# Kernel optimization log

Hardware: AMD Instinct MI355X
Metric: run time of the kernel (lower is better)

Reference implementation:

```python
import jax, jax.numpy as jnp
import numpy as np

SIGMA = 2.0
EPS = 1e-06
# Truncation radius for the distance transform. exp(-R^2/(2*sigma^2)) = exp(-128)
# underflows to 0.0 in float32, so clipping distances at R reproduces
# scipy.ndimage.distance_transform_edt -> exp(...) exactly in float32.
R = 32


def _boundary_weights(y, sigma=SIGMA, radius=R):
    """y: (B,H,W) binary {0,1}. Returns exp(-d^2/(2 sigma^2)) where d is the
    Euclidean distance to the nearest foreground pixel (0 on FG), computed by
    an exact two-pass separable EDT truncated at `radius` (exact in fp32 after exp)."""
    B, H, W = y.shape
    fg = y > 0.5
    Rf = jnp.float32(radius)
    offs = jnp.arange(-radius, radius + 1)

    # Pass 1 (vertical): g[i,j] = min(radius, min_{i': fg[i',j]} |i-i'|)
    fg_pad = jnp.pad(fg, ((0, 0), (radius, radius), (0, 0)))  # pad with False

    def vstep(g, o):
        sl = jax.lax.dynamic_slice_in_dim(fg_pad, radius + o, H, axis=1)
        g = jnp.minimum(g, jnp.where(sl, jnp.abs(o).astype(jnp.float32), Rf))
        return g, None

    g, _ = jax.lax.scan(vstep, jnp.full((B, H, W), Rf), offs)

    # Pass 2 (horizontal): d2[i,j] = min(radius^2, min_o g[i,j+o]^2 + o^2)
    g2 = g * g
    r2 = float(radius * radius)
    g2_pad = jnp.pad(g2, ((0, 0), (0, 0), (radius, radius)), constant_values=r2)

    def hstep(d2, o):
        sl = jax.lax.dynamic_slice_in_dim(g2_pad, radius + o, W, axis=2)
        d2 = jnp.minimum(d2, sl + (o * o).astype(jnp.float32))
        return d2, None

    d2, _ = jax.lax.scan(hstep, jnp.full((B, H, W), jnp.float32(r2)), offs)
    return jnp.exp(-d2 / (2.0 * sigma * sigma))


def setup_inputs() -> dict:
    key = jax.random.key(0)
    k1, k2 = jax.random.split(key)
    B, C, H, W = 8, 1, 1024, 1024
    probs = jax.random.uniform(k1, (B, C, H, W), dtype=jnp.float32,
                               minval=1e-4, maxval=1.0 - 1e-4)
    targets = (jax.random.uniform(k2, (B, C, H, W)) < 0.02).astype(jnp.float32)
    return {"probs": probs, "targets": targets}


def reference(probs, targets):
    eps = EPS
    y = (targets > 0.5).astype(probs.dtype)                      # (B,1,H,W)
    S_pos = y.sum()
    S_tot = float(y.size)
    S_neg = S_tot - S_pos
    w_pos = jnp.minimum((S_neg + eps) / (S_pos + eps), 1.0)      # scalar
    w_neg_base = (S_pos + eps) / (S_neg + eps)                   # scalar
    w_bdry = _boundary_weights(y[:, 0])[:, None]                 # (B,1,H,W)
    w_neg = jnp.minimum(w_neg_base + w_bdry, 1.0)
    p = jnp.clip(probs, eps, 1.0 - eps)
    loss = w_neg * (1.0 - y) * (-jnp.log1p(-p)) + w_pos * y * (-jnp.log(p))
    return loss.mean()
```

## Files before the change

kernel.cpp:

```cpp
#include <hip/hip_runtime.h>
#include <stdint.h>

#define BB 8
#define HH 1024
#define WW 1024
#define NPIXF 8388608.0f
#define TH 8
#define SROWS 24
#define NRB (HH / TH)
#define NBLK (NRB * BB)
#define GROW 292


__device__ __forceinline__ int phys_idx(int y) { return y + (y >> 3); }

__global__ __launch_bounds__(256, 4) void main_kernel(
    const float* __restrict__ probs,
    const float* __restrict__ targets,
    float4* __restrict__ ws4)
{
    __shared__ uint32_t fgb[SROWS][33];
    __shared__ uint32_t gtw[TH][GROW];
    __shared__ uint32_t redc[4];
    __shared__ float redf[4][3];

    const int t = threadIdx.x;
    const int v = t >> 6, l = t & 63;

    const int L = blockIdx.x + (blockIdx.y << 7);
    const int rb = ((L & 7) << 4) | ((L >> 3) & 15);
    const int b = L >> 7;
    const int r0 = rb * TH;
    const size_t ibase = (size_t)b << 20;

    const uint32_t* tg = (const uint32_t*)(targets + ibase);
    uint32_t cnt = 0;
    #pragma unroll
    for (int q = 0; q < 3; ++q) {
        const int task = q * 256 + t;
        const int r  = task >> 5;
        const int hw = task & 31;
        const int gr = r0 - 8 + r;
        uint32_t w = 0;
        if (gr >= 0 && gr < HH) {
            const uint4* rp = (const uint4*)(tg + ((size_t)gr << 10)) + (hw << 3);
            #pragma unroll
            for (int m = 0; m < 8; ++m) {
                const uint4 u = rp[m];
                const uint32_t nib = ((u.x >> 23) & 1u) | (((u.y >> 23) & 1u) << 1)
                                   | (((u.z >> 23) & 1u) << 2) | (((u.w >> 23) & 1u) << 3);
                w |= nib << (m << 2);
            }
        }
        fgb[r][hw] = w;
        if ((unsigned)(r - 8) < (unsigned)TH) cnt += __popc(w);
    }
    if (t < TH) {
        gtw[t][0] = 0x40404040u; gtw[t][1] = 0x40404040u;
        gtw[t][290] = 0x40404040u; gtw[t][291] = 0x40404040u;
    }
    __syncthreads();

    {
        const int i  = t >> 5;
        const int hw = t & 31;
        uint32_t rbw[15];
        #pragma unroll
        for (int s = 0; s < 15; ++s) rbw[s] = fgb[1 + i + s][hw];
        uint32_t D = rbw[7];
        uint32_t S0 = ~D, S1 = 0, S2 = 0, S3 = 0;
        #pragma unroll
        for (int k = 1; k <= 7; ++k) {
            D |= rbw[7 - k] | rbw[7 + k];
            const uint32_t cc = ~D;
            const uint32_t t0 = S0 & cc; S0 ^= cc;
            const uint32_t t1 = S1 & t0; S1 ^= t0;
            const uint32_t t2 = S2 & t1; S2 ^= t1;
            S3 |= t2;
        }
        #pragma unroll
        for (int m = 0; m < 8; ++m) {
            uint32_t pk = 0;
            #pragma unroll
            for (int c = 0; c < 4; ++c) {
                const int j = (m << 2) | c;
                const uint32_t g = ((S0 >> j) & 1u) | (((S1 >> j) & 1u) << 1)
                                 | (((S2 >> j) & 1u) << 2) | (((S3 >> j) & 1u) << 3);
                pk |= (g * g) << (c << 3);
            }
            const int y = 2 + (hw << 3) + m;
            gtw[i][phys_idx(y)] = pk;
        }
    }
    __syncthreads();

    uint32_t wv[TH][5];
    #pragma unroll
    for (int i = 0; i < TH; ++i) {
        #pragma unroll
        for (int k = 0; k < 5; ++k) wv[i][k] = gtw[i][phys_idx(t + k)];
    }

    float accA = 0.0f, accB = 0.0f, accC = 0.0f;
    const float4* pb = (const float4*)(probs + ibase) + ((size_t)r0 << 8);
    float4 pr = pb[t];
    #pragma unroll
    for (int i = 0; i < TH; ++i) {
        const float4 cur = pr;
        if (i + 1 < TH) pr = pb[((i + 1) << 8) + t];

        int sqb[19];
        #pragma unroll
        for (int rbx = 1; rbx <= 18; ++rbx)
            sqb[rbx] = (int)((wv[i][rbx >> 2] >> ((rbx & 3) << 3)) & 0xFFu);

        const float pv[4] = {cur.x, cur.y, cur.z, cur.w};
        #pragma unroll
        for (int cc = 0; cc < 4; ++cc) {
            int d2 = 64;
            #pragma unroll
            for (int m = 0; m < 15; ++m) {
                const int oc = (m - 7) * (m - 7);
                d2 = min(d2, sqb[cc + m + 1] + oc);
            }
            const float p = pv[cc];
            const bool y = (sqb[cc + 8] == 0);
            const float q = y ? p : (1.0f - p);
            const float L2 = -__logf(q);
            const float wb = __expf(-0.125f * (float)d2);
            const float Lbg = y ? 0.0f : L2;
            accA += (L2 - Lbg);
            accB += Lbg;
            accC = fmaf(wb, Lbg, accC);
        }
    }

    #pragma unroll
    for (int off = 32; off; off >>= 1) {
        accA += __shfl_down(accA, off, 64);
        accB += __shfl_down(accB, off, 64);
        accC += __shfl_down(accC, off, 64);
        cnt  += __shfl_down(cnt,  off, 64);
    }
    if (l == 0) { redc[v] = cnt; redf[v][0] = accA; redf[v][1] = accB; redf[v][2] = accC; }
    __syncthreads();
    if (t == 0) {
        float4 o;
        o.x = (float)(redc[0] + redc[1] + redc[2] + redc[3]);
        o.y = redf[0][0] + redf[1][0] + redf[2][0] + redf[3][0];
        o.z = redf[0][1] + redf[1][1] + redf[2][1] + redf[3][1];
        o.w = redf[0][2] + redf[1][2] + redf[2][2] + redf[3][2];
        ws4[b * NRB + rb] = o;
    }
}

__global__ __launch_bounds__(256) void final_kernel(
    const float4* __restrict__ ws4,
    float* __restrict__ out)
{
    __shared__ float4 red[4];
    const int t = threadIdx.x;
    float4 s = ws4[t];
    #pragma unroll
    for (int k = 1; k < NBLK / 256; ++k) {
        const float4 s2 = ws4[t + k * 256];
        s.x += s2.x; s.y += s2.y; s.z += s2.z; s.w += s2.w;
    }
    #pragma unroll
    for (int off = 32; off; off >>= 1) {
        s.x += __shfl_down(s.x, off, 64);
        s.y += __shfl_down(s.y, off, 64);
        s.z += __shfl_down(s.z, off, 64);
        s.w += __shfl_down(s.w, off, 64);
    }
    if ((t & 63) == 0) red[t >> 6] = s;
    __syncthreads();
    if (t == 0) {
        float4 a = red[0];
        #pragma unroll
        for (int k = 1; k < 4; ++k) {
            a.x += red[k].x; a.y += red[k].y; a.z += red[k].z; a.w += red[k].w;
        }
        const float S_pos = a.x;
        const float S_neg = NPIXF - S_pos;
        const float w_pos = fminf((S_neg + 1e-6f) / (S_pos + 1e-6f), 1.0f);
        const float w_negb = (S_pos + 1e-6f) / (S_neg + 1e-6f);
        out[0] = (w_pos * a.y + w_negb * a.z + a.w) / NPIXF;
    }
}

extern "C" void kernel_launch(void* const* d_in, const int* in_sizes, int n_in,
                              void* d_out, int out_size, void* d_ws, size_t ws_size,
                              hipStream_t stream) {
    const float* probs   = (const float*)d_in[0];
    const float* targets = (const float*)d_in[1];
    float4* ws4 = (float4*)d_ws;

    main_kernel<<<dim3(NRB, BB), 256, 0, stream>>>(probs, targets, ws4);
    final_kernel<<<1, 256, 0, stream>>>(ws4, (float*)d_out);
}
```

Measured before the change: 102.9 us.

## Split each row tile into two column halves and prefetch probs up front

Each block now handles an 8-row by 512-column tile instead of full rows, with a 32-column halo loaded from the targets on each side. This doubles the grid to 2048 blocks, raises the launch-bounds occupancy hint to 8 blocks per CU and shrinks shared memory per block. All four probs float4 loads are issued at kernel start, before the mask load, so they overlap with the EDT setup. The cost is redundant halo loads of targets and bit-packing, plus some idle threads in the vertical pass.

```diff
diff --git a/kernel.cpp b/kernel.cpp
--- a/kernel.cpp
+++ b/kernel.cpp
@@ -6,67 +6,81 @@
 #define WW 1024
 #define NPIXF 8388608.0f
 #define TH 8
+#define CW 512
 #define SROWS 24
+#define SHW 18
 #define NRB (HH / TH)
-#define NBLK (NRB * BB)
-#define GROW 292
+#define NCB (WW / CW)
+#define NBLK (NRB * NCB * BB)
+#define GROW2 164
 
 
 __device__ __forceinline__ int phys_idx(int y) { return y + (y >> 3); }
 
-__global__ __launch_bounds__(256, 4) void main_kernel(
+__global__ __launch_bounds__(256, 8) void main_kernel(
     const float* __restrict__ probs,
     const float* __restrict__ targets,
     float4* __restrict__ ws4)
 {
-    __shared__ uint32_t fgb[SROWS][33];
-    __shared__ uint32_t gtw[TH][GROW];
+    __shared__ uint32_t fgb[SROWS][SHW + 1];
+    __shared__ uint32_t gtw[TH][GROW2];
     __shared__ uint32_t redc[4];
     __shared__ float redf[4][3];
 
     const int t = threadIdx.x;
     const int v = t >> 6, l = t & 63;
 
-    const int L = blockIdx.x + (blockIdx.y << 7);
-    const int rb = ((L & 7) << 4) | ((L >> 3) & 15);
-    const int b = L >> 7;
+    const int bx = blockIdx.x;
+    const int xcd = bx & 7;
+    const int s = bx >> 3;
+    const int rb = (xcd << 4) | (s >> 1);
+    const int cb = s & 1;
+    const int b = blockIdx.y;
     const int r0 = rb * TH;
+    const int c0 = cb * CW;
     const size_t ibase = (size_t)b << 20;
+
+    const float4* pbase = (const float4*)(probs + ibase + ((size_t)r0 << 10) + c0);
+    const int i0 = t >> 7;
+    const int tc = t & 127;
+    float4 pr[4];
+    #pragma unroll
+    for (int it = 0; it < 4; ++it) pr[it] = pbase[((i0 + (it << 1)) << 8) + tc];
 
     const uint32_t* tg = (const uint32_t*)(targets + ibase);
     uint32_t cnt = 0;
     #pragma unroll
-    for (int q = 0; q < 3; ++q) {
+    for (int q = 0; q < 2; ++q) {
         const int task = q * 256 + t;
-        const int r  = task >> 5;
-        const int hw = task & 31;
-        const int gr = r0 - 8 + r;
-        uint32_t w = 0;
-        if (gr >= 0 && gr < HH) {
-            const uint4* rp = (const uint4*)(tg + ((size_t)gr << 10)) + (hw << 3);
-            #pragma unroll
-            for (int m = 0; m < 8; ++m) {
-                const uint4 u = rp[m];
-                const uint32_t nib = ((u.x >> 23) & 1u) | (((u.y >> 23) & 1u) << 1)
-                                   | (((u.z >> 23) & 1u) << 2) | (((u.w >> 23) & 1u) << 3);
-                w |= nib << (m << 2);
+        if (task < SROWS * SHW) {
+            const int r = task / SHW;
+            const int w = task - r * SHW;
+            const int gr = r0 - 8 + r;
+            const int cbase = c0 - 32 + (w << 5);
+            uint32_t wd = 0;
+            if (gr >= 0 && gr < HH && cbase >= 0 && cbase < WW) {
+                const uint4* rp = (const uint4*)(tg + ((size_t)gr << 10) + cbase);
+                #pragma unroll
+                for (int m = 0; m < 8; ++m) {
+                    const uint4 u = rp[m];
+                    const uint32_t nib = ((u.x >> 23) & 1u) | (((u.y >> 23) & 1u) << 1)
+                                       | (((u.z >> 23) & 1u) << 2) | (((u.w >> 23) & 1u) << 3);
+                    wd |= nib << (m << 2);
+                }
             }
-        }
-        fgb[r][hw] = w;
-        if ((unsigned)(r - 8) < (unsigned)TH) cnt += __popc(w);
-    }
-    if (t < TH) {
-        gtw[t][0] = 0x40404040u; gtw[t][1] = 0x40404040u;
-        gtw[t][290] = 0x40404040u; gtw[t][291] = 0x40404040u;
-    }
-    __syncthreads();
-
-    {
-        const int i  = t >> 5;
-        const int hw = t & 31;
+            fgb[r][w] = wd;
+            if ((unsigned)(r - 8) < (unsigned)TH && (unsigned)(w - 1) < 16u)
+                cnt += __popc(wd);
+        }
+    }
+    __syncthreads();
+
+    if (t < TH * SHW) {
+        const int i = t / SHW;
+        const int w = t - i * SHW;
         uint32_t rbw[15];
         #pragma unroll
-        for (int s = 0; s < 15; ++s) rbw[s] = fgb[1 + i + s][hw];
+        for (int s2 = 0; s2 < 15; ++s2) rbw[s2] = fgb[1 + i + s2][w];
         uint32_t D = rbw[7];
         uint32_t S0 = ~D, S1 = 0, S2 = 0, S3 = 0;
         #pragma unroll
@@ -88,33 +102,28 @@
                                  | (((S2 >> j) & 1u) << 2) | (((S3 >> j) & 1u) << 3);
                 pk |= (g * g) << (c << 3);
             }
-            const int y = 2 + (hw << 3) + m;
-            gtw[i][phys_idx(y)] = pk;
-        }
-    }
-    __syncthreads();
-
-    uint32_t wv[TH][5];
-    #pragma unroll
-    for (int i = 0; i < TH; ++i) {
-        #pragma unroll
-        for (int k = 0; k < 5; ++k) wv[i][k] = gtw[i][phys_idx(t + k)];
+            gtw[i][9 * w + m] = pk;
+        }
+    }
+    __syncthreads();
+
+    uint32_t wv[4][5];
+    #pragma unroll
+    for (int it = 0; it < 4; ++it) {
+        const int i = i0 + (it << 1);
+        #pragma unroll
+        for (int k = 0; k < 5; ++k) wv[it][k] = gtw[i][phys_idx(tc + 6 + k)];
     }
 
     float accA = 0.0f, accB = 0.0f, accC = 0.0f;
-    const float4* pb = (const float4*)(probs + ibase) + ((size_t)r0 << 8);
-    float4 pr = pb[t];
-    #pragma unroll
-    for (int i = 0; i < TH; ++i) {
-        const float4 cur = pr;
-        if (i + 1 < TH) pr = pb[((i + 1) << 8) + t];
-
+    #pragma unroll
+    for (int it = 0; it < 4; ++it) {
         int sqb[19];
         #pragma unroll
         for (int rbx = 1; rbx <= 18; ++rbx)
-            sqb[rbx] = (int)((wv[i][rbx >> 2] >> ((rbx & 3) << 3)) & 0xFFu);
-
-        const float pv[4] = {cur.x, cur.y, cur.z, cur.w};
+            sqb[rbx] = (int)((wv[it][rbx >> 2] >> ((rbx & 3) << 3)) & 0xFFu);
+
+        const float pv[4] = {pr[it].x, pr[it].y, pr[it].z, pr[it].w};
         #pragma unroll
         for (int cc = 0; cc < 4; ++cc) {
             int d2 = 64;
@@ -150,7 +159,7 @@
         o.y = redf[0][0] + redf[1][0] + redf[2][0] + redf[3][0];
         o.z = redf[0][1] + redf[1][1] + redf[2][1] + redf[3][1];
         o.w = redf[0][2] + redf[1][2] + redf[2][2] + redf[3][2];
-        ws4[b * NRB + rb] = o;
+        ws4[(b << 8) + (rb << 1) + cb] = o;
     }
 }
 
@@ -196,6 +205,6 @@
     const float* targets = (const float*)d_in[1];
     float4* ws4 = (float4*)d_ws;
 
-    main_kernel<<<dim3(NRB, BB), 256, 0, stream>>>(probs, targets, ws4);
+    main_kernel<<<dim3(NRB * NCB, BB), 256, 0, stream>>>(probs, targets, ws4);
     final_kernel<<<1, 256, 0, stream>>>(ws4, (float*)d_out);
 }
```

After: 104.1 us. About the same (+1.1%).
